# Performance work log

Measured on AMD Instinct MI355X. Metric: run time of the kernel, lower is better.

Reference implementation:

```python
import jax, jax.numpy as jnp
import numpy as np

VOCAB = 50000
EMBED = 128
CONTENT = 200
HIDDEN = 1024
LABELS = 2
BATCH = 4096


def setup_inputs() -> dict:
    key = jax.random.key(0)
    k_x, k_emb, k_w1, k_b1, k_w2, k_b2 = jax.random.split(key, 6)
    x = jax.random.randint(k_x, (BATCH, CONTENT), 0, VOCAB, dtype=jnp.int64)
    emb_table = jax.random.normal(k_emb, (VOCAB, EMBED), dtype=jnp.float32)
    fan_in1 = EMBED * CONTENT
    w1 = jax.random.uniform(k_w1, (HIDDEN, fan_in1), dtype=jnp.float32,
                            minval=-1.0, maxval=1.0) / np.sqrt(fan_in1)
    b1 = jax.random.uniform(k_b1, (HIDDEN,), dtype=jnp.float32,
                            minval=-1.0, maxval=1.0) / np.sqrt(fan_in1)
    w2 = jax.random.uniform(k_w2, (LABELS, HIDDEN), dtype=jnp.float32,
                            minval=-1.0, maxval=1.0) / np.sqrt(HIDDEN)
    b2 = jax.random.uniform(k_b2, (LABELS,), dtype=jnp.float32,
                            minval=-1.0, maxval=1.0) / np.sqrt(HIDDEN)
    return {"x": x, "emb_table": emb_table, "w1": w1, "b1": b1,
            "w2": w2, "b2": b2}


def reference(x, emb_table, w1, b1, w2, b2):
    # padding_idx=0: row 0 of the embedding table is zero
    table = emb_table.at[0].set(0.0)
    emb = table[x]                                   # [B, C, E]
    flat = emb.reshape(emb.shape[0], -1)             # [B, C*E]
    h = jax.nn.relu(flat @ w1.T + b1)                # [B, H]
    logits = h @ w2.T + b2                           # [B, L]
    # Softmax(dim=0) on a 1-D per-sample vector == softmax over labels
    return jax.nn.softmax(logits, axis=-1)
```

## Files before the change

### kernel.cpp

```cpp
#include <hip/hip_runtime.h>
#include <hip/hip_bf16.h>
#include <stdint.h>

#define BATCH   4096
#define CONTENT 200
#define EMBED   128
#define HIDDEN  1024
#define KDIM    (CONTENT*EMBED)
#define SPLITK  4

typedef __bf16 bf16_t;
typedef __bf16 bf16x8 __attribute__((ext_vector_type(8)));
typedef float  f32x4  __attribute__((ext_vector_type(4)));

#define WS_EMBT  0ull
#define WS_W1    12800000ull
#define WS_HP    65228800ull
#define HP_STRIDE 4194304ull

__device__ __forceinline__ void gload_lds16(const void* g, void* l) {
  __builtin_amdgcn_global_load_lds(
      (const __attribute__((address_space(1))) uint32_t*)g,
      (__attribute__((address_space(3))) uint32_t*)l, 16, 0, 0);
}

__global__ __launch_bounds__(256) void k_prep(const float* __restrict__ emb,
                                              const float* __restrict__ w1,
                                              bf16_t* __restrict__ embT,
                                              bf16_t* __restrict__ w1T) {
  if (blockIdx.x < 320) {
    const int NU = 800000;
    int stride = 320 * 256;
    for (int u = blockIdx.x * 256 + threadIdx.x; u < NU; u += stride) {
      const float4* s = (const float4*)(emb + (size_t)u * 8);
      float4 f0 = s[0], f1 = s[1];
      float sc = (u >> 4) == 0 ? 0.0f : 1.0f;
      bf16x8 r;
      r[0]=(bf16_t)(f0.x*sc); r[1]=(bf16_t)(f0.y*sc); r[2]=(bf16_t)(f0.z*sc); r[3]=(bf16_t)(f0.w*sc);
      r[4]=(bf16_t)(f1.x*sc); r[5]=(bf16_t)(f1.y*sc); r[6]=(bf16_t)(f1.z*sc); r[7]=(bf16_t)(f1.w*sc);
      *(bf16x8*)(embT + (size_t)u * 8) = r;
    }
  } else {
    const long long NU = 3276800;
    long long stride = 2048LL * 256;
    for (long long u = (long long)(blockIdx.x - 320) * 256 + threadIdx.x; u < NU; u += stride) {
      const float4* s = (const float4*)(w1 + u * 8);
      float4 f0 = s[0], f1 = s[1];
      bf16x8 r;
      r[0]=(bf16_t)f0.x; r[1]=(bf16_t)f0.y; r[2]=(bf16_t)f0.z; r[3]=(bf16_t)f0.w;
      r[4]=(bf16_t)f1.x; r[5]=(bf16_t)f1.y; r[6]=(bf16_t)f1.z; r[7]=(bf16_t)f1.w;
      *(bf16x8*)(w1T + u * 8) = r;
    }
  }
}

__global__ __launch_bounds__(512, 2) void k_gemm(const int* __restrict__ x,
                                                 const bf16_t* __restrict__ embT,
                                                 const bf16_t* __restrict__ W,
                                                 float* __restrict__ hp) {
  __shared__ char smem[131072];
  const int tid = threadIdx.x;
  const int wid = tid >> 6, l = tid & 63;
  const int orig = (blockIdx.x & 7) * 32 + (blockIdx.x >> 3);
  const int m0 = (orig & 15) * 256;
  const int n0 = ((orig >> 4) & 3) * 256;
  const int chunk = orig >> 6;
  const int cb100 = chunk * 100;
  const int T0 = chunk * 50;

  const int sg16 = ((l & 7) ^ (l >> 3)) * 16;
  const char* embB = (const char*)embT;
  const char* Wb = (const char*)W;
  const int wq = wid >> 2, wm = wid & 3;
  size_t brow[2];
  #pragma unroll
  for (int rd = 0; rd < 2; ++rd)
    brow[rd] = (size_t)(n0 + rd*128 + wq*64 + wm*8 + (l>>3)) * (size_t)(KDIM*2) + sg16;
  int xrow[4];
  #pragma unroll
  for (int f = 0; f < 4; ++f)
    xrow[f] = (m0 + (f>>1)*128 + (f&1)*64 + (tid>>3)) * CONTENT;

  const int wr = wq, wc = wm;
  const int lane_r = l & 15, g = l >> 4;
  const int aoff = wr*16384 + lane_r*128;
  const int boff = 32768 + wc*8192 + lane_r*128;
  const int s0 = ((0*4 + g) ^ (lane_r & 7)) * 16;
  const int s1 = ((1*4 + g) ^ (lane_r & 7)) * 16;

#define ISSUE_A(BUF, H, XA, KOFF)                                             \
  { gload_lds16(embB + (size_t)XA[0*2+(H)]*256 + (KOFF) + sg16,               \
                smem + (BUF) + 0*16384 + (H)*8192 + wid*1024);                \
    gload_lds16(embB + (size_t)XA[1*2+(H)]*256 + (KOFF) + sg16,               \
                smem + (BUF) + 1*16384 + (H)*8192 + wid*1024); }
#define ISSUE_B(BUF, H, LT)                                                   \
  { const int lt_ = (LT) > 99 ? 99 : (LT);                                    \
    const size_t ko_ = (size_t)(cb100 + lt_) * 128 + (H)*1638400u;            \
    gload_lds16(Wb + brow[0] + ko_,                                           \
                smem + (BUF) + 32768 + 0*16384 + wq*8192 + (H)*4096 + wm*1024); \
    gload_lds16(Wb + brow[1] + ko_,                                           \
                smem + (BUF) + 32768 + 1*16384 + wq*8192 + (H)*4096 + wm*1024); }

#define PHASE(IH, JH, CB, ISSUE_STMT, TAIL)                                   \
  { bf16x8 af[4][2], bfr[2][2];                                               \
    _Pragma("unroll")                                                         \
    for (int ii = 0; ii < 4; ++ii) {                                          \
      af[ii][0] = *(const bf16x8*)(smem + (CB) + aoff + (IH)*8192 + ii*2048 + s0); \
      af[ii][1] = *(const bf16x8*)(smem + (CB) + aoff + (IH)*8192 + ii*2048 + s1); \
    }                                                                         \
    _Pragma("unroll")                                                         \
    for (int jj = 0; jj < 2; ++jj) {                                          \
      bfr[jj][0] = *(const bf16x8*)(smem + (CB) + boff + (JH)*4096 + jj*2048 + s0); \
      bfr[jj][1] = *(const bf16x8*)(smem + (CB) + boff + (JH)*4096 + jj*2048 + s1); \
    }                                                                         \
    ISSUE_STMT                                                                \
    __builtin_amdgcn_s_barrier();                                             \
    asm volatile("s_waitcnt lgkmcnt(0)" ::: "memory");                        \
    __builtin_amdgcn_s_setprio(1);                                            \
    _Pragma("unroll")                                                         \
    for (int ii = 0; ii < 4; ++ii)                                            \
      _Pragma("unroll")                                                       \
      for (int jj = 0; jj < 2; ++jj) {                                        \
        acc[(IH)*4+ii][(JH)*2+jj] = __builtin_amdgcn_mfma_f32_16x16x32_bf16(  \
            af[ii][0], bfr[jj][0], acc[(IH)*4+ii][(JH)*2+jj], 0, 0, 0);       \
        acc[(IH)*4+ii][(JH)*2+jj] = __builtin_amdgcn_mfma_f32_16x16x32_bf16(  \
            af[ii][1], bfr[jj][1], acc[(IH)*4+ii][(JH)*2+jj], 0, 0, 0);       \
      }                                                                       \
    __builtin_amdgcn_s_setprio(0);                                            \
    TAIL                                                                      \
    __builtin_amdgcn_s_barrier(); }

  f32x4 acc[8][4];
  #pragma unroll
  for (int i = 0; i < 8; ++i)
    #pragma unroll
    for (int j = 0; j < 4; ++j)
      acc[i][j] = (f32x4){0.f, 0.f, 0.f, 0.f};

  int xcur[4], xnxt[4];
  #pragma unroll
  for (int f = 0; f < 4; ++f) xcur[f] = x[xrow[f] + T0];
  #pragma unroll
  for (int f = 0; f < 4; ++f) xnxt[f] = x[xrow[f] + T0 + 1];
  ISSUE_A(0, 0, xcur, 0)
  ISSUE_A(0, 1, xcur, 0)
  ISSUE_B(0, 0, 0)
  ISSUE_B(0, 1, 0)
  ISSUE_A(65536, 0, xcur, 128)
  ISSUE_B(65536, 0, 1)
  asm volatile("s_waitcnt vmcnt(4)" ::: "memory");
  __builtin_amdgcn_s_barrier();

  for (int j = 0; j < 50; ++j) {
    int tnew = T0 + j + 2; if (tnew > CONTENT - 1) tnew = CONTENT - 1;
    int xnew[4];
    #pragma unroll
    for (int f = 0; f < 4; ++f) xnew[f] = x[xrow[f] + tnew];

    PHASE(0,0, 0,     { ISSUE_A(65536, 1, xcur, 128); }, {})
    PHASE(0,1, 0,     { ISSUE_B(65536, 1, 2*j+1); }, {})
    PHASE(1,0, 0,     { ISSUE_A(0, 0, xnxt, 0); }, {})
    PHASE(1,1, 0,     { ISSUE_B(0, 0, 2*j+2); },
                      { asm volatile("s_waitcnt vmcnt(4)" ::: "memory"); })
    PHASE(0,0, 65536, { ISSUE_A(0, 1, xnxt, 0); }, {})
    PHASE(0,1, 65536, { ISSUE_B(0, 1, 2*j+2); }, {})
    PHASE(1,0, 65536, { ISSUE_A(65536, 0, xnxt, 128); }, {})
    PHASE(1,1, 65536, { ISSUE_B(65536, 0, 2*j+3); },
                      { asm volatile("s_waitcnt vmcnt(4)" ::: "memory"); })

    #pragma unroll
    for (int f = 0; f < 4; ++f) { xcur[f] = xnxt[f]; xnxt[f] = xnew[f]; }
  }
#undef PHASE
#undef ISSUE_A
#undef ISSUE_B

  asm volatile("s_waitcnt vmcnt(0)" ::: "memory");

  float* hout = hp + (size_t)chunk * HP_STRIDE;
  const int colBase = n0 + wc * 64 + lane_r;
  const int rowBase = m0 + wr * 128 + (l >> 4) * 4;
  #pragma unroll
  for (int i = 0; i < 8; ++i)
    #pragma unroll
    for (int jj = 0; jj < 4; ++jj)
      #pragma unroll
      for (int r = 0; r < 4; ++r)
        hout[(size_t)(rowBase + i * 16 + r) * HIDDEN + colBase + jj * 16] = acc[i][jj][r];
}

__global__ __launch_bounds__(256) void k_final(const float* __restrict__ hp,
                                               const float* __restrict__ b1,
                                               const float* __restrict__ w2,
                                               const float* __restrict__ b2,
                                               float* __restrict__ out) {
  const int tid = threadIdx.x;
  const int w = tid >> 6, l = tid & 63;
  const int m = blockIdx.x * 4 + w;
  const float* r0 = hp + (size_t)m * HIDDEN;
  const float* r1 = r0 + HP_STRIDE;
  const float* r2 = r1 + HP_STRIDE;
  const float* r3 = r2 + HP_STRIDE;
  float l0 = 0.f, l1 = 0.f;
  #pragma unroll
  for (int t = 0; t < 4; ++t) {
    int j = t * 256 + l * 4;
    float4 p0 = *(const float4*)(r0 + j);
    float4 p1 = *(const float4*)(r1 + j);
    float4 p2 = *(const float4*)(r2 + j);
    float4 p3 = *(const float4*)(r3 + j);
    float4 bb = *(const float4*)(b1 + j);
    float4 wa = *(const float4*)(w2 + j);
    float4 wb = *(const float4*)(w2 + HIDDEN + j);
    float h;
    h = p0.x + p1.x + p2.x + p3.x + bb.x; h = fmaxf(h, 0.f); l0 += h * wa.x; l1 += h * wb.x;
    h = p0.y + p1.y + p2.y + p3.y + bb.y; h = fmaxf(h, 0.f); l0 += h * wa.y; l1 += h * wb.y;
    h = p0.z + p1.z + p2.z + p3.z + bb.z; h = fmaxf(h, 0.f); l0 += h * wa.z; l1 += h * wb.z;
    h = p0.w + p1.w + p2.w + p3.w + bb.w; h = fmaxf(h, 0.f); l0 += h * wa.w; l1 += h * wb.w;
  }
  #pragma unroll
  for (int off = 32; off > 0; off >>= 1) {
    l0 += __shfl_xor(l0, off, 64);
    l1 += __shfl_xor(l1, off, 64);
  }
  if (l == 0) {
    float z0 = l0 + b2[0], z1 = l1 + b2[1];
    float mx = fmaxf(z0, z1);
    float e0 = expf(z0 - mx), e1 = expf(z1 - mx);
    float s = 1.f / (e0 + e1);
    out[2 * m]     = e0 * s;
    out[2 * m + 1] = e1 * s;
  }
}

extern "C" void kernel_launch(void* const* d_in, const int* in_sizes, int n_in,
                              void* d_out, int out_size, void* d_ws, size_t ws_size,
                              hipStream_t stream) {
  (void)in_sizes; (void)n_in; (void)out_size; (void)ws_size;
  const int*   x   = (const int*)d_in[0];
  const float* emb = (const float*)d_in[1];
  const float* w1  = (const float*)d_in[2];
  const float* b1  = (const float*)d_in[3];
  const float* w2  = (const float*)d_in[4];
  const float* b2  = (const float*)d_in[5];
  float* out = (float*)d_out;
  char* ws = (char*)d_ws;
  bf16_t* embT = (bf16_t*)(ws + WS_EMBT);
  bf16_t* Wbf  = (bf16_t*)(ws + WS_W1);
  float*  hp   = (float*)(ws + WS_HP);

  hipLaunchKernelGGL(k_prep,  dim3(2368), dim3(256), 0, stream, emb, w1, embT, Wbf);
  hipLaunchKernelGGL(k_gemm,  dim3(256), dim3(512), 0, stream, x, embT, Wbf, hp);
  hipLaunchKernelGGL(k_final, dim3(BATCH/4), dim3(256), 0, stream, hp, b1, w2, b2, out);
}
```

Baseline: 391.6 us.

## Fuse final reduction into GEMM via per-row-block counter, reorder MFMA phases for fragment reuse

```diff
diff --git a/kernel.cpp b/kernel.cpp
--- a/kernel.cpp
+++ b/kernel.cpp
@@ -18,6 +18,8 @@
 #define WS_HP    65228800ull
 #define HP_STRIDE 4194304ull
 
+__device__ int g_cnt[16];
+
 __device__ __forceinline__ void gload_lds16(const void* g, void* l) {
   __builtin_amdgcn_global_load_lds(
       (const __attribute__((address_space(1))) uint32_t*)g,
@@ -28,10 +30,11 @@
                                               const float* __restrict__ w1,
                                               bf16_t* __restrict__ embT,
                                               bf16_t* __restrict__ w1T) {
-  if (blockIdx.x < 320) {
-    const int NU = 800000;
-    int stride = 320 * 256;
-    for (int u = blockIdx.x * 256 + threadIdx.x; u < NU; u += stride) {
+  if (blockIdx.x == 0 && threadIdx.x < 16) g_cnt[threadIdx.x] = 0;
+  const int TOT = 4076800;
+  int stride = gridDim.x * 256;
+  for (int u = blockIdx.x * 256 + threadIdx.x; u < TOT; u += stride) {
+    if (u < 800000) {
       const float4* s = (const float4*)(emb + (size_t)u * 8);
       float4 f0 = s[0], f1 = s[1];
       float sc = (u >> 4) == 0 ? 0.0f : 1.0f;
@@ -39,17 +42,14 @@
       r[0]=(bf16_t)(f0.x*sc); r[1]=(bf16_t)(f0.y*sc); r[2]=(bf16_t)(f0.z*sc); r[3]=(bf16_t)(f0.w*sc);
       r[4]=(bf16_t)(f1.x*sc); r[5]=(bf16_t)(f1.y*sc); r[6]=(bf16_t)(f1.z*sc); r[7]=(bf16_t)(f1.w*sc);
       *(bf16x8*)(embT + (size_t)u * 8) = r;
-    }
-  } else {
-    const long long NU = 3276800;
-    long long stride = 2048LL * 256;
-    for (long long u = (long long)(blockIdx.x - 320) * 256 + threadIdx.x; u < NU; u += stride) {
-      const float4* s = (const float4*)(w1 + u * 8);
+    } else {
+      long long v = u - 800000;
+      const float4* s = (const float4*)(w1 + v * 8);
       float4 f0 = s[0], f1 = s[1];
       bf16x8 r;
       r[0]=(bf16_t)f0.x; r[1]=(bf16_t)f0.y; r[2]=(bf16_t)f0.z; r[3]=(bf16_t)f0.w;
       r[4]=(bf16_t)f1.x; r[5]=(bf16_t)f1.y; r[6]=(bf16_t)f1.z; r[7]=(bf16_t)f1.w;
-      *(bf16x8*)(w1T + u * 8) = r;
+      *(bf16x8*)(w1T + v * 8) = r;
     }
   }
 }
@@ -57,7 +57,11 @@
 __global__ __launch_bounds__(512, 2) void k_gemm(const int* __restrict__ x,
                                                  const bf16_t* __restrict__ embT,
                                                  const bf16_t* __restrict__ W,
-                                                 float* __restrict__ hp) {
+                                                 float* __restrict__ hp,
+                                                 const float* __restrict__ b1,
+                                                 const float* __restrict__ w2,
+                                                 const float* __restrict__ b2,
+                                                 float* __restrict__ out) {
   __shared__ char smem[131072];
   const int tid = threadIdx.x;
   const int wid = tid >> 6, l = tid & 63;
@@ -101,33 +105,53 @@
     gload_lds16(Wb + brow[1] + ko_,                                           \
                 smem + (BUF) + 32768 + 1*16384 + wq*8192 + (H)*4096 + wm*1024); }
 
-#define PHASE(IH, JH, CB, ISSUE_STMT, TAIL)                                   \
-  { bf16x8 af[4][2], bfr[2][2];                                               \
-    _Pragma("unroll")                                                         \
-    for (int ii = 0; ii < 4; ++ii) {                                          \
-      af[ii][0] = *(const bf16x8*)(smem + (CB) + aoff + (IH)*8192 + ii*2048 + s0); \
-      af[ii][1] = *(const bf16x8*)(smem + (CB) + aoff + (IH)*8192 + ii*2048 + s1); \
-    }                                                                         \
-    _Pragma("unroll")                                                         \
-    for (int jj = 0; jj < 2; ++jj) {                                          \
-      bfr[jj][0] = *(const bf16x8*)(smem + (CB) + boff + (JH)*4096 + jj*2048 + s0); \
-      bfr[jj][1] = *(const bf16x8*)(smem + (CB) + boff + (JH)*4096 + jj*2048 + s1); \
-    }                                                                         \
-    ISSUE_STMT                                                                \
-    __builtin_amdgcn_s_barrier();                                             \
-    asm volatile("s_waitcnt lgkmcnt(0)" ::: "memory");                        \
-    __builtin_amdgcn_s_setprio(1);                                            \
-    _Pragma("unroll")                                                         \
-    for (int ii = 0; ii < 4; ++ii)                                            \
-      _Pragma("unroll")                                                       \
-      for (int jj = 0; jj < 2; ++jj) {                                        \
-        acc[(IH)*4+ii][(JH)*2+jj] = __builtin_amdgcn_mfma_f32_16x16x32_bf16(  \
-            af[ii][0], bfr[jj][0], acc[(IH)*4+ii][(JH)*2+jj], 0, 0, 0);       \
-        acc[(IH)*4+ii][(JH)*2+jj] = __builtin_amdgcn_mfma_f32_16x16x32_bf16(  \
-            af[ii][1], bfr[jj][1], acc[(IH)*4+ii][(JH)*2+jj], 0, 0, 0);       \
-      }                                                                       \
-    __builtin_amdgcn_s_setprio(0);                                            \
-    TAIL                                                                      \
+#define MM8(AF, BF, IB, JB)                                                   \
+  _Pragma("unroll") for (int ii = 0; ii < 4; ++ii)                            \
+    _Pragma("unroll") for (int jj = 0; jj < 2; ++jj) {                        \
+      acc[(IB)+ii][(JB)+jj] = __builtin_amdgcn_mfma_f32_16x16x32_bf16(        \
+          AF[ii][0], BF[jj][0], acc[(IB)+ii][(JB)+jj], 0, 0, 0);              \
+      acc[(IB)+ii][(JB)+jj] = __builtin_amdgcn_mfma_f32_16x16x32_bf16(        \
+          AF[ii][1], BF[jj][1], acc[(IB)+ii][(JB)+jj], 0, 0, 0);              \
+    }
+
+#define RD_AF(DST, CB, H)                                                     \
+  _Pragma("unroll") for (int ii = 0; ii < 4; ++ii) {                          \
+    DST[ii][0] = *(const bf16x8*)(smem + (CB) + aoff + (H)*8192 + ii*2048 + s0); \
+    DST[ii][1] = *(const bf16x8*)(smem + (CB) + aoff + (H)*8192 + ii*2048 + s1); \
+  }
+#define RD_BF(DST, CB, H)                                                     \
+  _Pragma("unroll") for (int jj = 0; jj < 2; ++jj) {                          \
+    DST[jj][0] = *(const bf16x8*)(smem + (CB) + boff + (H)*4096 + jj*2048 + s0); \
+    DST[jj][1] = *(const bf16x8*)(smem + (CB) + boff + (H)*4096 + jj*2048 + s1); \
+  }
+
+#define BARW  __builtin_amdgcn_s_barrier();                                   \
+              asm volatile("s_waitcnt lgkmcnt(0)" ::: "memory");
+
+#define TILE(CB, ST1, ST2, ST3, ST4, TAIL4)                                   \
+  { RD_AF(af0, CB, 0) RD_BF(bf0, CB, 0)                                       \
+    ST1                                                                       \
+    BARW                                                                      \
+    __builtin_amdgcn_s_setprio(1); MM8(af0, bf0, 0, 0)                        \
+    __builtin_amdgcn_s_setprio(0);                                            \
+    __builtin_amdgcn_s_barrier();                                             \
+    RD_BF(bf1, CB, 1)                                                         \
+    ST2                                                                       \
+    BARW                                                                      \
+    __builtin_amdgcn_s_setprio(1); MM8(af0, bf1, 0, 2)                        \
+    __builtin_amdgcn_s_setprio(0);                                            \
+    __builtin_amdgcn_s_barrier();                                             \
+    RD_AF(af1, CB, 1)                                                         \
+    ST3                                                                       \
+    BARW                                                                      \
+    __builtin_amdgcn_s_setprio(1); MM8(af1, bf1, 4, 2)                        \
+    __builtin_amdgcn_s_setprio(0);                                            \
+    __builtin_amdgcn_s_barrier();                                             \
+    ST4                                                                       \
+    __builtin_amdgcn_s_barrier();                                             \
+    __builtin_amdgcn_s_setprio(1); MM8(af1, bf0, 4, 0)                        \
+    __builtin_amdgcn_s_setprio(0);                                            \
+    TAIL4                                                                     \
     __builtin_amdgcn_s_barrier(); }
 
   f32x4 acc[8][4];
@@ -136,6 +160,8 @@
     #pragma unroll
     for (int j = 0; j < 4; ++j)
       acc[i][j] = (f32x4){0.f, 0.f, 0.f, 0.f};
+
+  bf16x8 af0[4][2], af1[4][2], bf0[2][2], bf1[2][2];
 
   int xcur[4], xnxt[4];
   #pragma unroll
@@ -157,21 +183,27 @@
     #pragma unroll
     for (int f = 0; f < 4; ++f) xnew[f] = x[xrow[f] + tnew];
 
-    PHASE(0,0, 0,     { ISSUE_A(65536, 1, xcur, 128); }, {})
-    PHASE(0,1, 0,     { ISSUE_B(65536, 1, 2*j+1); }, {})
-    PHASE(1,0, 0,     { ISSUE_A(0, 0, xnxt, 0); }, {})
-    PHASE(1,1, 0,     { ISSUE_B(0, 0, 2*j+2); },
-                      { asm volatile("s_waitcnt vmcnt(4)" ::: "memory"); })
-    PHASE(0,0, 65536, { ISSUE_A(0, 1, xnxt, 0); }, {})
-    PHASE(0,1, 65536, { ISSUE_B(0, 1, 2*j+2); }, {})
-    PHASE(1,0, 65536, { ISSUE_A(65536, 0, xnxt, 128); }, {})
-    PHASE(1,1, 65536, { ISSUE_B(65536, 0, 2*j+3); },
-                      { asm volatile("s_waitcnt vmcnt(4)" ::: "memory"); })
+    TILE(0,
+         { ISSUE_A(65536, 1, xcur, 128); },
+         { ISSUE_B(65536, 1, 2*j+1); },
+         { ISSUE_A(0, 0, xnxt, 0); },
+         { ISSUE_B(0, 0, 2*j+2); },
+         { asm volatile("s_waitcnt vmcnt(4)" ::: "memory"); })
+    TILE(65536,
+         { ISSUE_A(0, 1, xnxt, 0); },
+         { ISSUE_B(0, 1, 2*j+2); },
+         { ISSUE_A(65536, 0, xnxt, 128); },
+         { ISSUE_B(65536, 0, 2*j+3); },
+         { asm volatile("s_waitcnt vmcnt(4)" ::: "memory"); })
 
     #pragma unroll
     for (int f = 0; f < 4; ++f) { xcur[f] = xnxt[f]; xnxt[f] = xnew[f]; }
   }
-#undef PHASE
+#undef TILE
+#undef BARW
+#undef RD_AF
+#undef RD_BF
+#undef MM8
 #undef ISSUE_A
 #undef ISSUE_B
 
@@ -187,31 +219,31 @@
       #pragma unroll
       for (int r = 0; r < 4; ++r)
         hout[(size_t)(rowBase + i * 16 + r) * HIDDEN + colBase + jj * 16] = acc[i][jj][r];
-}
-
-__global__ __launch_bounds__(256) void k_final(const float* __restrict__ hp,
-                                               const float* __restrict__ b1,
-                                               const float* __restrict__ w2,
-                                               const float* __restrict__ b2,
-                                               float* __restrict__ out) {
-  const int tid = threadIdx.x;
-  const int w = tid >> 6, l = tid & 63;
-  const int m = blockIdx.x * 4 + w;
-  const float* r0 = hp + (size_t)m * HIDDEN;
-  const float* r1 = r0 + HP_STRIDE;
-  const float* r2 = r1 + HP_STRIDE;
-  const float* r3 = r2 + HP_STRIDE;
+
+  __threadfence();
+  const int m0i = orig & 15;
+  __syncthreads();
+  if (tid == 0) {
+    atomicAdd(&g_cnt[m0i], 1);
+    while (atomicAdd(&g_cnt[m0i], 0) < 16) __builtin_amdgcn_s_sleep(8);
+  }
+  __syncthreads();
+  __threadfence();
+
+  const int rank = orig >> 4;
+  const int mrow = m0 + rank * 16 + (tid >> 5);
+  const int c0 = (tid & 31) * 32;
+  const float* h0 = hp + (size_t)mrow * HIDDEN + c0;
   float l0 = 0.f, l1 = 0.f;
   #pragma unroll
-  for (int t = 0; t < 4; ++t) {
-    int j = t * 256 + l * 4;
-    float4 p0 = *(const float4*)(r0 + j);
-    float4 p1 = *(const float4*)(r1 + j);
-    float4 p2 = *(const float4*)(r2 + j);
-    float4 p3 = *(const float4*)(r3 + j);
-    float4 bb = *(const float4*)(b1 + j);
-    float4 wa = *(const float4*)(w2 + j);
-    float4 wb = *(const float4*)(w2 + HIDDEN + j);
+  for (int q = 0; q < 8; ++q) {
+    float4 p0 = *(const float4*)(h0 + q * 4);
+    float4 p1 = *(const float4*)(h0 + HP_STRIDE + q * 4);
+    float4 p2 = *(const float4*)(h0 + 2 * HP_STRIDE + q * 4);
+    float4 p3 = *(const float4*)(h0 + 3 * HP_STRIDE + q * 4);
+    float4 bb = *(const float4*)(b1 + c0 + q * 4);
+    float4 wa = *(const float4*)(w2 + c0 + q * 4);
+    float4 wb = *(const float4*)(w2 + HIDDEN + c0 + q * 4);
     float h;
     h = p0.x + p1.x + p2.x + p3.x + bb.x; h = fmaxf(h, 0.f); l0 += h * wa.x; l1 += h * wb.x;
     h = p0.y + p1.y + p2.y + p3.y + bb.y; h = fmaxf(h, 0.f); l0 += h * wa.y; l1 += h * wb.y;
@@ -219,17 +251,17 @@
     h = p0.w + p1.w + p2.w + p3.w + bb.w; h = fmaxf(h, 0.f); l0 += h * wa.w; l1 += h * wb.w;
   }
   #pragma unroll
-  for (int off = 32; off > 0; off >>= 1) {
+  for (int off = 16; off > 0; off >>= 1) {
     l0 += __shfl_xor(l0, off, 64);
     l1 += __shfl_xor(l1, off, 64);
   }
-  if (l == 0) {
+  if ((tid & 31) == 0) {
     float z0 = l0 + b2[0], z1 = l1 + b2[1];
     float mx = fmaxf(z0, z1);
     float e0 = expf(z0 - mx), e1 = expf(z1 - mx);
     float s = 1.f / (e0 + e1);
-    out[2 * m]     = e0 * s;
-    out[2 * m + 1] = e1 * s;
+    out[2 * mrow]     = e0 * s;
+    out[2 * mrow + 1] = e1 * s;
   }
 }
 
@@ -249,7 +281,7 @@
   bf16_t* Wbf  = (bf16_t*)(ws + WS_W1);
   float*  hp   = (float*)(ws + WS_HP);
 
-  hipLaunchKernelGGL(k_prep,  dim3(2368), dim3(256), 0, stream, emb, w1, embT, Wbf);
-  hipLaunchKernelGGL(k_gemm,  dim3(256), dim3(512), 0, stream, x, embT, Wbf, hp);
-  hipLaunchKernelGGL(k_final, dim3(BATCH/4), dim3(256), 0, stream, hp, b1, w2, b2, out);
-}
+  hipLaunchKernelGGL(k_prep, dim3(2048), dim3(256), 0, stream, emb, w1, embT, Wbf);
+  hipLaunchKernelGGL(k_gemm, dim3(256), dim3(512), 0, stream,
+                     x, embT, Wbf, hp, b1, w2, b2, out);
+}
```

Result: slower. 513.4 us (+31.1%).
